# Optimization experiments

Hardware: AMD Instinct MI355X
Metric: run time of the kernel (lower is better)

Reference implementation:

```python
import jax, jax.numpy as jnp
import numpy as np

MARGIN = 1.0
N, D = 8192, 128
NUM_CLASSES = 1024


def setup_inputs() -> dict:
    key = jax.random.key(0)
    k1, k2, k3 = jax.random.split(key, 3)
    a = jax.random.normal(k1, (N, D), dtype=jnp.float32)
    b = jax.random.normal(k2, (N, D), dtype=jnp.float32)
    # L2-normalize embeddings (standard for metric learning; keeps exp() stable)
    a = a / jnp.linalg.norm(a, axis=1, keepdims=True)
    b = b / jnp.linalg.norm(b, axis=1, keepdims=True)
    labels = jax.random.randint(k3, (N,), 0, NUM_CLASSES, dtype=jnp.int64 if jax.config.jax_enable_x64 else jnp.int32)
    return {"a": a, "b": b, "labels": labels}


def reference(a, b, labels):
    # S[i, j] = a_i . b_j  -- full pairwise similarity, one GEMM
    S = a @ b.T  # [N, N]
    same = labels[:, None] == labels[None, :]  # [N, N]
    eye = jnp.eye(labels.shape[0], dtype=bool)
    pos_mask = same & ~eye          # ordered positive pairs (i != j, same label)
    neg_mask = ~same                # ordered negative pairs (labels differ)
    # V[i] = sum_k in neg(i) exp(margin + S[i, k])
    V = jnp.sum(jnp.where(neg_mask, jnp.exp(MARGIN + S), 0.0), axis=1)  # [N]
    # per positive pair (i, j): max(log(V_i + V_j) - S_ij, 0)^2
    hinge = jnp.maximum(jnp.log(V[:, None] + V[None, :]) - S, 0.0)
    comp = jnp.where(pos_mask, hinge * hinge, 0.0)
    num_pos = jnp.sum(pos_mask)
    loss = jnp.sum(comp) / (2.0 * num_pos.astype(S.dtype))
    return loss
```

## Files before the change

kernel.cpp:

```cpp
#include <hip/hip_runtime.h>

#define NN 8192
#define DD 128
#define MAXCLS 64
#define NCHUNK 8
#define NBLK 512
#define LOG2E 1.4426950408889634f
#define E1    2.718281828459045f

typedef __attribute__((ext_vector_type(8))) short bf16x8;
typedef __attribute__((ext_vector_type(4))) float f32x4;

#if __has_builtin(__builtin_amdgcn_exp2f)
#define EXP2F(x) __builtin_amdgcn_exp2f(x)
#else
#define EXP2F(x) exp2f(x)
#endif

__device__ __forceinline__ void load16_lds(const unsigned short* g, unsigned short* l) {
    __builtin_amdgcn_global_load_lds(
        (const __attribute__((address_space(1))) unsigned int*)g,
        (__attribute__((address_space(3))) unsigned int*)l,
        16, 0, 0);
}

__device__ __forceinline__ unsigned short f2bf(float x) {
    unsigned u = __float_as_uint(x);
    u = (u + 0x7FFFu + ((u >> 16) & 1u)) >> 16;
    return (unsigned short)u;
}

__device__ __forceinline__ void st_agent(float* p, float v) {
    __hip_atomic_store(p, v, __ATOMIC_RELAXED, __HIP_MEMORY_SCOPE_AGENT);
}
__device__ __forceinline__ void st_agent(int* p, int v) {
    __hip_atomic_store(p, v, __ATOMIC_RELAXED, __HIP_MEMORY_SCOPE_AGENT);
}
__device__ __forceinline__ void st_agent(unsigned int* p, unsigned int v) {
    __hip_atomic_store(p, v, __ATOMIC_RELAXED, __HIP_MEMORY_SCOPE_AGENT);
}
__device__ __forceinline__ void st_agent(unsigned long long* p, unsigned long long v) {
    __hip_atomic_store(p, v, __ATOMIC_RELAXED, __HIP_MEMORY_SCOPE_AGENT);
}
__device__ __forceinline__ unsigned int ld_agent(const unsigned int* p) {
    return __hip_atomic_load(p, __ATOMIC_RELAXED, __HIP_MEMORY_SCOPE_AGENT);
}

__device__ __forceinline__ int xcd_id() {
    return (int)(__builtin_amdgcn_s_getreg(20 | (0 << 6) | (31 << 11)) & 7u);
}

__device__ __forceinline__ void grid_sync(int* subcnt, int* root, unsigned int* gen,
                                          unsigned int* doneg, int relay, int myxcd,
                                          int sub) {
    __syncthreads();
    if (threadIdx.x == 0) {
        unsigned int g = ld_agent(gen);
        int v = __hip_atomic_fetch_add(&subcnt[sub * 32], 1,
                                       __ATOMIC_RELAXED, __HIP_MEMORY_SCOPE_AGENT);
        if (v == (NBLK / 8) - 1) {
            __hip_atomic_store(&subcnt[sub * 32], 0, __ATOMIC_RELAXED, __HIP_MEMORY_SCOPE_AGENT);
            int r = __hip_atomic_fetch_add(root, 1, __ATOMIC_RELAXED, __HIP_MEMORY_SCOPE_AGENT);
            if (r == 7) {
                __hip_atomic_store(root, 0, __ATOMIC_RELAXED, __HIP_MEMORY_SCOPE_AGENT);
                st_agent(gen, g + 1u);
            }
        }
        if (relay) {
            long long t0 = clock64();
            while (ld_agent(gen) == g) {
                __builtin_amdgcn_s_sleep(1);
                if (clock64() - t0 > (1LL << 24)) break;
            }
            st_agent(&doneg[myxcd * 32], g + 1u);
        } else {
            long long t1 = clock64();
            while ((int)(ld_agent(&doneg[myxcd * 32]) - (g + 1u)) < 0) {
                __builtin_amdgcn_s_sleep(1);
                if (clock64() - t1 > (1LL << 24)) break;
            }
        }
    }
    __syncthreads();
}

__global__ __launch_bounds__(256, 2) void ml_fused_kernel(
    const float* __restrict__ a, const float* __restrict__ b,
    const int* __restrict__ labels,
    unsigned short* __restrict__ abf, unsigned short* __restrict__ bbf,
    int* __restrict__ cnt, int* __restrict__ list,
    float* __restrict__ Vp,
    float* __restrict__ classLoss, int* __restrict__ classCnt,
    float* __restrict__ out,
    int* subcnt, int* root, unsigned int* gen,
    int* claim, unsigned int* doneg)
{
    __shared__ unsigned short Bs[2][128 * DD];
    __shared__ float red[2][64];

    const int tid = threadIdx.x;
    const int bid = blockIdx.x;
    const int sub = bid & 7;

    int relay = 0, myxcd = 0;
    if (tid == 0) {
        myxcd = xcd_id();
        relay = (__hip_atomic_fetch_add(&claim[myxcd * 32], 1,
                                        __ATOMIC_RELAXED, __HIP_MEMORY_SCOPE_AGENT) == 0);
    }

#pragma unroll
    for (int it = 0; it < 4; it++) {
        int t = it * (NBLK * 256) + bid * 256 + tid;
        const float* src = a;
        unsigned short* dst = abf;
        int idx = t;
        float scale = LOG2E;
        if (t >= 262144) { src = b; dst = bbf; idx = t - 262144; scale = 1.0f; }
        float4 v = ((const float4*)src)[idx];
        ushort4 o;
        o.x = f2bf(v.x * scale); o.y = f2bf(v.y * scale);
        o.z = f2bf(v.z * scale); o.w = f2bf(v.w * scale);
        union { ushort4 v4; unsigned long long u; } cvt;
        cvt.v4 = o;
        st_agent(((unsigned long long*)dst) + idx, cvt.u);
        if (t < NN) {
            int c = labels[t];
            int p = atomicAdd(&cnt[c], 1);
            if (p < MAXCLS) st_agent(&list[c * MAXCLS + p], t);
        }
    }

    grid_sync(subcnt, root, gen, doneg, relay, myxcd, sub);

    {
        const int lane = tid & 63;
        const int wv   = tid >> 6;
        const int row0 = (bid >> 3) * 128;
        const int j0   = (bid & 7) * 1024;

        const int lr = lane >> 4;
        const int sp = lane & 15;
        const int m  = lane & 15;
        const int q  = lane >> 4;
        const int xr = m & 7;

#pragma unroll
        for (int i = 0; i < 8; i++) {
            int rb = wv * 32 + i * 4;
            int r  = rb + lr;
            int cc = sp ^ (r & 7);
            load16_lds(&abf[(size_t)(row0 + r) * DD + cc * 8], &Bs[0][rb * DD]);
        }
#pragma unroll
        for (int i = 0; i < 8; i++) {
            int rb = wv * 32 + i * 4;
            int r  = rb + lr;
            int cc = sp ^ (r & 7);
            load16_lds(&bbf[(size_t)(j0 + r) * DD + cc * 8], &Bs[1][rb * DD]);
        }
        __syncthreads();

        const int wi = (wv >> 1) * 64;
        const int wj = (wv & 1) * 64;

        bf16x8 afr[4][4];
#pragma unroll
        for (int ti = 0; ti < 4; ti++)
#pragma unroll
            for (int ks = 0; ks < 4; ks++) {
                int r   = wi + ti * 16 + m;
                int pos = (ks * 4 + q) ^ xr;
                afr[ti][ks] = *(const bf16x8*)(&Bs[0][r * DD + pos * 8]);
            }
        asm volatile("s_waitcnt lgkmcnt(0)" ::: "memory");
        __syncthreads();

#pragma unroll
        for (int i = 0; i < 8; i++) {
            int rb = wv * 32 + i * 4;
            int r  = rb + lr;
            int cc = sp ^ (r & 7);
            load16_lds(&bbf[(size_t)(j0 + 128 + r) * DD + cc * 8], &Bs[0][rb * DD]);
        }

        float rs[4][4];
#pragma unroll
        for (int ti = 0; ti < 4; ti++)
#pragma unroll
            for (int rg = 0; rg < 4; rg++) rs[ti][rg] = 0.f;

        const f32x4 zero = {0.f, 0.f, 0.f, 0.f};
        f32x4 acc[4][4];

#define COMPUTE_TILE(BUF)                                                              \
        {                                                                              \
            __builtin_amdgcn_s_setprio(1);                                             \
            _Pragma("unroll")                                                          \
            for (int ks = 0; ks < 4; ks++) {                                           \
                bf16x8 bfr[4];                                                         \
                _Pragma("unroll")                                                      \
                for (int tj = 0; tj < 4; tj++) {                                       \
                    int r   = wj + tj * 16 + m;                                        \
                    int pos = (ks * 4 + q) ^ xr;                                       \
                    bfr[tj] = *(const bf16x8*)(&Bs[BUF][r * DD + pos * 8]);            \
                }                                                                      \
                _Pragma("unroll")                                                      \
                for (int ti = 0; ti < 4; ti++)                                         \
                    _Pragma("unroll")                                                  \
                    for (int tj = 0; tj < 4; tj++)                                     \
                        acc[ti][tj] = __builtin_amdgcn_mfma_f32_16x16x32_bf16(         \
                            afr[ti][ks], bfr[tj], (ks == 0) ? zero : acc[ti][tj],      \
                            0, 0, 0);                                                  \
            }                                                                          \
            __builtin_amdgcn_s_setprio(0);                                             \
        }

#define STAGE_B(JT, BUF)                                                               \
        _Pragma("unroll")                                                              \
        for (int i = 0; i < 8; i++) {                                                  \
            int rb = wv * 32 + i * 4;                                                  \
            int r  = rb + lr;                                                          \
            int cc = sp ^ (r & 7);                                                     \
            load16_lds(&bbf[(size_t)(j0 + (JT) * 128 + r) * DD + cc * 8],              \
                       &Bs[BUF][rb * DD]);                                             \
        }

#define EPILOGUE()                                                                     \
        _Pragma("unroll")                                                              \
        for (int ti = 0; ti < 4; ti++)                                                 \
            _Pragma("unroll")                                                          \
            for (int tj = 0; tj < 4; tj++) {                                           \
                f32x4 c = acc[ti][tj];                                                 \
                rs[ti][0] += EXP2F(c[0]);                                              \
                rs[ti][1] += EXP2F(c[1]);                                              \
                rs[ti][2] += EXP2F(c[2]);                                              \
                rs[ti][3] += EXP2F(c[3]);                                              \
            }

#pragma unroll 2
        for (int jt = 0; jt < 6; jt++) {
            const int cb = (jt + 1) & 1;
            COMPUTE_TILE(cb);
            asm volatile("s_waitcnt lgkmcnt(0)" ::: "memory");
            __builtin_amdgcn_s_barrier();
            STAGE_B(jt + 2, cb);
            EPILOGUE();
            asm volatile("s_waitcnt vmcnt(8)" ::: "memory");
            __builtin_amdgcn_s_barrier();
        }
        {
            COMPUTE_TILE(1);
            EPILOGUE();
            asm volatile("s_waitcnt vmcnt(0)" ::: "memory");
            __builtin_amdgcn_s_barrier();
        }
        {
            COMPUTE_TILE(0);
            EPILOGUE();
        }

#undef COMPUTE_TILE
#undef STAGE_B
#undef EPILOGUE

#pragma unroll
        for (int ti = 0; ti < 4; ti++)
#pragma unroll
            for (int rg = 0; rg < 4; rg++) {
                float v = rs[ti][rg];
                v += __shfl_xor(v, 1);
                v += __shfl_xor(v, 2);
                v += __shfl_xor(v, 4);
                v += __shfl_xor(v, 8);
                rs[ti][rg] = v;
            }

        if ((wv & 1) == 1 && m == 0) {
#pragma unroll
            for (int ti = 0; ti < 4; ti++)
#pragma unroll
                for (int rg = 0; rg < 4; rg++)
                    red[wv >> 1][ti * 16 + q * 4 + rg] = rs[ti][rg];
        }
        __syncthreads();
        if ((wv & 1) == 0 && m == 0) {
#pragma unroll
            for (int ti = 0; ti < 4; ti++)
#pragma unroll
                for (int rg = 0; rg < 4; rg++) {
                    int rloc = ti * 16 + q * 4 + rg;
                    st_agent(&Vp[(size_t)(bid & 7) * NN + row0 + wi + rloc],
                             rs[ti][rg] + red[wv >> 1][rloc]);
                }
        }
    }

    grid_sync(subcnt, root, gen, doneg, relay, myxcd, sub);

    {
        char* sm = (char*)&Bs[0][0];
        const int h  = tid >> 7;
        const int ht = tid & 127;
        int*   mem    = (int*)  (sm + h * 18432);
        float* sumExp = (float*)(sm + h * 18432 + 256);
        float* Vadj   = (float*)(sm + h * 18432 + 512);
        float* Sc     = (float*)(sm + h * 18432 + 1024);
        float* ps     = (float*)(sm + h * 18432 + 17408);
        int*   cs     = (int*)  (sm + h * 18432 + 17424);

        const int c = bid * 2 + h;
        int mc = cnt[c];
        if (mc > MAXCLS) mc = MAXCLS;

        float vsum = 0.f;
        if (ht < mc) {
            int r = list[c * MAXCLS + ht];
            mem[ht] = r;
#pragma unroll
            for (int jc = 0; jc < NCHUNK; jc++) vsum += Vp[(size_t)jc * NN + r];
        }
        if (ht < MAXCLS) sumExp[ht] = 0.f;
        __syncthreads();

        const int g = ht >> 4;
        const int l = ht & 15;
        const int tot1 = mc * mc;
        for (int pp = g; pp < tot1; pp += 8) {
            int i = pp / mc;
            int j = pp - i * mc;
            int ri = mem[i], rj = mem[j];
            const float4* ar = (const float4*)(a + (size_t)ri * DD) + l * 2;
            const float4* br = (const float4*)(b + (size_t)rj * DD) + l * 2;
            float4 a0 = ar[0], a1 = ar[1];
            float4 b0 = br[0], b1 = br[1];
            float s = 0.f;
            s = fmaf(a0.x, b0.x, s); s = fmaf(a0.y, b0.y, s);
            s = fmaf(a0.z, b0.z, s); s = fmaf(a0.w, b0.w, s);
            s = fmaf(a1.x, b1.x, s); s = fmaf(a1.y, b1.y, s);
            s = fmaf(a1.z, b1.z, s); s = fmaf(a1.w, b1.w, s);
            s += __shfl_xor(s, 1);
            s += __shfl_xor(s, 2);
            s += __shfl_xor(s, 4);
            s += __shfl_xor(s, 8);
            if (l == 0) {
                Sc[i * MAXCLS + j] = s;
                atomicAdd(&sumExp[i], __expf(s));
            }
        }
        __syncthreads();

        if (ht < mc) Vadj[ht] = E1 * (vsum - sumExp[ht]);
        __syncthreads();

        float partial = 0.f;
        int   count   = 0;
        for (int pp = ht; pp < tot1; pp += 128) {
            int i = pp / mc;
            int j = pp - i * mc;
            if (i != j) {
                float hg = fmaxf(logf(Vadj[i] + Vadj[j]) - Sc[i * MAXCLS + j], 0.f);
                partial += hg * hg;
                count++;
            }
        }
        for (int off = 32; off > 0; off >>= 1) {
            partial += __shfl_down(partial, off);
            count   += __shfl_down(count, off);
        }
        if ((ht & 63) == 0) { ps[ht >> 6] = partial; cs[ht >> 6] = count; }
        __syncthreads();
        if (ht == 0) {
            st_agent(&classLoss[c], ps[0] + ps[1]);
            st_agent(&classCnt[c],  cs[0] + cs[1]);
        }
    }

    __syncthreads();
    __shared__ int amLast;
    if (tid == 0) {
        int last = 0;
        int v = __hip_atomic_fetch_add(&subcnt[sub * 32], 1,
                                       __ATOMIC_RELAXED, __HIP_MEMORY_SCOPE_AGENT);
        if (v == (NBLK / 8) - 1) {
            __hip_atomic_store(&subcnt[sub * 32], 0, __ATOMIC_RELAXED, __HIP_MEMORY_SCOPE_AGENT);
            int r = __hip_atomic_fetch_add(root, 1, __ATOMIC_RELAXED, __HIP_MEMORY_SCOPE_AGENT);
            if (r == 7) { __hip_atomic_store(root, 0, __ATOMIC_RELAXED, __HIP_MEMORY_SCOPE_AGENT); last = 1; }
        }
        amLast = last;
    }
    __syncthreads();
    if (amLast) {
        __shared__ double dred[4];
        __shared__ long long cred[4];
        const int lane = tid & 63, wvv = tid >> 6;
        double dls = 0.0;
        long long dct = 0;
        for (int k = tid; k < 1024; k += 256) {
            dls += (double)__hip_atomic_load(&classLoss[k], __ATOMIC_RELAXED, __HIP_MEMORY_SCOPE_AGENT);
            dct += (long long)__hip_atomic_load(&classCnt[k], __ATOMIC_RELAXED, __HIP_MEMORY_SCOPE_AGENT);
        }
        for (int off = 32; off > 0; off >>= 1) {
            dls += __shfl_down(dls, off);
            dct += __shfl_down(dct, off);
        }
        if (lane == 0) { dred[wvv] = dls; cred[wvv] = dct; }
        __syncthreads();
        if (tid == 0) {
            double ls = dred[0] + dred[1] + dred[2] + dred[3];
            long long np = cred[0] + cred[1] + cred[2] + cred[3];
            out[0] = (float)(ls / (2.0 * (double)np));
        }
    }
}

extern "C" void kernel_launch(void* const* d_in, const int* in_sizes, int n_in,
                              void* d_out, int out_size, void* d_ws, size_t ws_size,
                              hipStream_t stream)
{
    const float* a      = (const float*)d_in[0];
    const float* b      = (const float*)d_in[1];
    const int*   labels = (const int*)d_in[2];
    float* out = (float*)d_out;

    char* ws = (char*)d_ws;
    unsigned short* abf = (unsigned short*)ws;
    unsigned short* bbf = (unsigned short*)(ws + 2097152);
    char*     base2     = ws + 4194304;
    int*      cnt       = (int*)(base2);
    int*      subcnt    = (int*)(base2 + 4096);
    int*      root      = (int*)(base2 + 5120);
    unsigned int* gen   = (unsigned int*)(base2 + 5248);
    int*      claim     = (int*)(base2 + 5376);
    unsigned int* doneg = (unsigned int*)(base2 + 6400);
    float*    classLoss = (float*)(base2 + 8192);
    int*      classCnt  = (int*)(base2 + 12288);
    int*      list      = (int*)(base2 + 16384);
    float*    Vp        = (float*)(base2 + 278528);

    (void)hipMemsetAsync(cnt, 0, 8192, stream);

    ml_fused_kernel<<<NBLK, 256, 0, stream>>>(
        a, b, labels, abf, bbf, cnt, list, Vp, classLoss, classCnt, out,
        subcnt, root, gen, claim, doneg);
}
```

Baseline: 111.7 us.

## Double block size to 512 threads with 256-row A tiles sharing B stages

Halves the grid to 256 blocks of 512 threads, so each block computes a 256-row slab of the similarity matrix against the same staged B tiles. Eight waves now share each B tile loaded into LDS, which halves the B global traffic per output. Each wave keeps its 64 A rows in registers, loaded in two passes through one LDS buffer. The class-loss phase now has four classes per block. This adds barriers to A staging, and with launch bounds of two blocks per CU the register budget per thread gets tighter. It also leaves fewer blocks to spread across CUs.

```diff
diff --git a/kernel.cpp b/kernel.cpp
--- a/kernel.cpp
+++ b/kernel.cpp
@@ -4,7 +4,8 @@
 #define DD 128
 #define MAXCLS 64
 #define NCHUNK 8
-#define NBLK 512
+#define NBLK 256
+#define TPB  512
 #define LOG2E 1.4426950408889634f
 #define E1    2.718281828459045f
 
@@ -84,7 +85,7 @@
     __syncthreads();
 }
 
-__global__ __launch_bounds__(256, 2) void ml_fused_kernel(
+__global__ __launch_bounds__(TPB, 2) void ml_fused_kernel(
     const float* __restrict__ a, const float* __restrict__ b,
     const int* __restrict__ labels,
     unsigned short* __restrict__ abf, unsigned short* __restrict__ bbf,
@@ -95,8 +96,9 @@
     int* subcnt, int* root, unsigned int* gen,
     int* claim, unsigned int* doneg)
 {
-    __shared__ unsigned short Bs[2][128 * DD];
-    __shared__ float red[2][64];
+    __shared__ char SM[74240];
+    unsigned short (*Bs)[128 * DD] = (unsigned short (*)[128 * DD])SM;
+    float* red = (float*)(SM + 73728);
 
     const int tid = threadIdx.x;
     const int bid = blockIdx.x;
@@ -111,7 +113,7 @@
 
 #pragma unroll
     for (int it = 0; it < 4; it++) {
-        int t = it * (NBLK * 256) + bid * 256 + tid;
+        int t = it * (NBLK * TPB) + bid * TPB + tid;
         const float* src = a;
         unsigned short* dst = abf;
         int idx = t;
@@ -136,7 +138,7 @@
     {
         const int lane = tid & 63;
         const int wv   = tid >> 6;
-        const int row0 = (bid >> 3) * 128;
+        const int row0 = (bid >> 3) * 256;
         const int j0   = (bid & 7) * 1024;
 
         const int lr = lane >> 4;
@@ -145,44 +147,52 @@
         const int q  = lane >> 4;
         const int xr = m & 7;
 
-#pragma unroll
-        for (int i = 0; i < 8; i++) {
-            int rb = wv * 32 + i * 4;
-            int r  = rb + lr;
-            int cc = sp ^ (r & 7);
-            load16_lds(&abf[(size_t)(row0 + r) * DD + cc * 8], &Bs[0][rb * DD]);
-        }
-#pragma unroll
-        for (int i = 0; i < 8; i++) {
-            int rb = wv * 32 + i * 4;
-            int r  = rb + lr;
-            int cc = sp ^ (r & 7);
-            load16_lds(&bbf[(size_t)(j0 + r) * DD + cc * 8], &Bs[1][rb * DD]);
-        }
+#define STAGE128(SRCBASE, BUF)                                                         \
+        _Pragma("unroll")                                                              \
+        for (int i = 0; i < 4; i++) {                                                  \
+            int rb = wv * 16 + i * 4;                                                  \
+            int r  = rb + lr;                                                          \
+            int cc = sp ^ (r & 7);                                                     \
+            load16_lds(&(SRCBASE)[(size_t)r * DD + cc * 8], &Bs[BUF][rb * DD]);        \
+        }
+
+        STAGE128(&abf[(size_t)row0 * DD], 0);
+        STAGE128(&bbf[(size_t)j0 * DD], 1);
         __syncthreads();
 
         const int wi = (wv >> 1) * 64;
         const int wj = (wv & 1) * 64;
 
         bf16x8 afr[4][4];
-#pragma unroll
-        for (int ti = 0; ti < 4; ti++)
-#pragma unroll
-            for (int ks = 0; ks < 4; ks++) {
-                int r   = wi + ti * 16 + m;
-                int pos = (ks * 4 + q) ^ xr;
-                afr[ti][ks] = *(const bf16x8*)(&Bs[0][r * DD + pos * 8]);
-            }
+        if (wv < 4) {
+#pragma unroll
+            for (int ti = 0; ti < 4; ti++)
+#pragma unroll
+                for (int ks = 0; ks < 4; ks++) {
+                    int r   = wi + ti * 16 + m;
+                    int pos = (ks * 4 + q) ^ xr;
+                    afr[ti][ks] = *(const bf16x8*)(&Bs[0][r * DD + pos * 8]);
+                }
+        }
         asm volatile("s_waitcnt lgkmcnt(0)" ::: "memory");
         __syncthreads();
 
-#pragma unroll
-        for (int i = 0; i < 8; i++) {
-            int rb = wv * 32 + i * 4;
-            int r  = rb + lr;
-            int cc = sp ^ (r & 7);
-            load16_lds(&bbf[(size_t)(j0 + 128 + r) * DD + cc * 8], &Bs[0][rb * DD]);
-        }
+        STAGE128(&abf[(size_t)(row0 + 128) * DD], 0);
+        __syncthreads();
+        if (wv >= 4) {
+#pragma unroll
+            for (int ti = 0; ti < 4; ti++)
+#pragma unroll
+                for (int ks = 0; ks < 4; ks++) {
+                    int r   = (wi - 128) + ti * 16 + m;
+                    int pos = (ks * 4 + q) ^ xr;
+                    afr[ti][ks] = *(const bf16x8*)(&Bs[0][r * DD + pos * 8]);
+                }
+        }
+        asm volatile("s_waitcnt lgkmcnt(0)" ::: "memory");
+        __syncthreads();
+
+        STAGE128(&bbf[(size_t)(j0 + 128) * DD], 0);
 
         float rs[4][4];
 #pragma unroll
@@ -216,16 +226,6 @@
             __builtin_amdgcn_s_setprio(0);                                             \
         }
 
-#define STAGE_B(JT, BUF)                                                               \
-        _Pragma("unroll")                                                              \
-        for (int i = 0; i < 8; i++) {                                                  \
-            int rb = wv * 32 + i * 4;                                                  \
-            int r  = rb + lr;                                                          \
-            int cc = sp ^ (r & 7);                                                     \
-            load16_lds(&bbf[(size_t)(j0 + (JT) * 128 + r) * DD + cc * 8],              \
-                       &Bs[BUF][rb * DD]);                                             \
-        }
-
 #define EPILOGUE()                                                                     \
         _Pragma("unroll")                                                              \
         for (int ti = 0; ti < 4; ti++)                                                 \
@@ -244,9 +244,9 @@
             COMPUTE_TILE(cb);
             asm volatile("s_waitcnt lgkmcnt(0)" ::: "memory");
             __builtin_amdgcn_s_barrier();
-            STAGE_B(jt + 2, cb);
+            STAGE128(&bbf[(size_t)(j0 + (jt + 2) * 128) * DD], cb);
             EPILOGUE();
-            asm volatile("s_waitcnt vmcnt(8)" ::: "memory");
+            asm volatile("s_waitcnt vmcnt(4)" ::: "memory");
             __builtin_amdgcn_s_barrier();
         }
         {
@@ -261,7 +261,7 @@
         }
 
 #undef COMPUTE_TILE
-#undef STAGE_B
+#undef STAGE128
 #undef EPILOGUE
 
 #pragma unroll
@@ -281,7 +281,7 @@
             for (int ti = 0; ti < 4; ti++)
 #pragma unroll
                 for (int rg = 0; rg < 4; rg++)
-                    red[wv >> 1][ti * 16 + q * 4 + rg] = rs[ti][rg];
+                    red[(wv >> 1) * 64 + ti * 16 + q * 4 + rg] = rs[ti][rg];
         }
         __syncthreads();
         if ((wv & 1) == 0 && m == 0) {
@@ -291,7 +291,7 @@
                 for (int rg = 0; rg < 4; rg++) {
                     int rloc = ti * 16 + q * 4 + rg;
                     st_agent(&Vp[(size_t)(bid & 7) * NN + row0 + wi + rloc],
-                             rs[ti][rg] + red[wv >> 1][rloc]);
+                             rs[ti][rg] + red[(wv >> 1) * 64 + rloc]);
                 }
         }
     }
@@ -299,7 +299,7 @@
     grid_sync(subcnt, root, gen, doneg, relay, myxcd, sub);
 
     {
-        char* sm = (char*)&Bs[0][0];
+        char* sm = (char*)SM;
         const int h  = tid >> 7;
         const int ht = tid & 127;
         int*   mem    = (int*)  (sm + h * 18432);
@@ -309,7 +309,7 @@
         float* ps     = (float*)(sm + h * 18432 + 17408);
         int*   cs     = (int*)  (sm + h * 18432 + 17424);
 
-        const int c = bid * 2 + h;
+        const int c = bid * 4 + h;
         int mc = cnt[c];
         if (mc > MAXCLS) mc = MAXCLS;
 
@@ -391,12 +391,12 @@
     }
     __syncthreads();
     if (amLast) {
-        __shared__ double dred[4];
-        __shared__ long long cred[4];
+        __shared__ double dred[8];
+        __shared__ long long cred[8];
         const int lane = tid & 63, wvv = tid >> 6;
         double dls = 0.0;
         long long dct = 0;
-        for (int k = tid; k < 1024; k += 256) {
+        for (int k = tid; k < 1024; k += TPB) {
             dls += (double)__hip_atomic_load(&classLoss[k], __ATOMIC_RELAXED, __HIP_MEMORY_SCOPE_AGENT);
             dct += (long long)__hip_atomic_load(&classCnt[k], __ATOMIC_RELAXED, __HIP_MEMORY_SCOPE_AGENT);
         }
@@ -407,8 +407,10 @@
         if (lane == 0) { dred[wvv] = dls; cred[wvv] = dct; }
         __syncthreads();
         if (tid == 0) {
-            double ls = dred[0] + dred[1] + dred[2] + dred[3];
-            long long np = cred[0] + cred[1] + cred[2] + cred[3];
+            double ls = 0.0;
+            long long np = 0;
+#pragma unroll
+            for (int w = 0; w < 8; w++) { ls += dred[w]; np += cred[w]; }
             out[0] = (float)(ls / (2.0 * (double)np));
         }
     }
@@ -440,7 +442,7 @@
 
     (void)hipMemsetAsync(cnt, 0, 8192, stream);
 
-    ml_fused_kernel<<<NBLK, 256, 0, stream>>>(
+    ml_fused_kernel<<<NBLK, TPB, 0, stream>>>(
         a, b, labels, abf, bbf, cnt, list, Vp, classLoss, classCnt, out,
         subcnt, root, gen, claim, doneg);
 }
```

Result: no change. 112.4 us (+0.6%).
